# Performance work log

Measured on AMD Instinct MI355X. Metric: run time of the kernel, lower is better.

Reference implementation:

```python
import jax, jax.numpy as jnp
import numpy as np

B, C, H, W = 8, 64, 128, 128
NH, OPH = 4, 16
MX, MY = 32, 17  # n_modes=(32,32) -> modes_y = 32//2+1
NPAT_S, NPAT_F = 10000, 5000
ED_S, ED_F = 64, 32


def setup_inputs() -> dict:
    ks = jax.random.split(jax.random.key(0), 16)
    n = lambda k, s, sc=1.0: jax.random.normal(k, s, dtype=jnp.float32) * sc
    z = lambda s: jnp.zeros(s, jnp.float32)
    return dict(
        x=n(ks[0], (B, C, H, W)),
        se_emb=n(ks[1], (NPAT_S, ED_S)),
        se_w=n(ks[2], (ED_S, C), 0.1), se_b=z(C),
        mhf_wr=n(ks[3], (NH, C, OPH, MX, MY), 0.01),
        mhf_wi=n(ks[4], (NH, C, OPH, MX, MY), 0.01),
        mhf_bias=z(C),
        sp_emb=n(ks[5], (NPAT_F, ED_F)),
        sp_wr=n(ks[6], (ED_F, C * MX * MY), 0.05), sp_br=z(C * MX * MY),
        sp_wi=n(ks[7], (ED_F, C * MX * MY), 0.05), sp_bi=z(C * MX * MY),
        gate_w1=n(ks[8], (3 * C, 64), 0.05), gate_b1=z(64),
        gate_w2=n(ks[9], (64, 3), 0.05), gate_b2=z(3),
        skip_w=n(ks[10], (C, C), 0.05), skip_b=z(C),
        norm_g=jnp.ones(C), norm_b=z(C),
        mlp_w1=n(ks[11], (C, 2 * C), 0.05), mlp_b1=z(2 * C),
        mlp_w2=n(ks[12], (2 * C, C), 0.05), mlp_b2=z(C),
    )


def _gelu(v):
    return jax.nn.gelu(v, approximate=False)


def _block(x, se_emb, se_w, se_b, mhf_wr, mhf_wi, mhf_bias, sp_emb, sp_wr, sp_br,
           sp_wi, sp_bi, gate_w1, gate_b1, gate_w2, gate_b2, skip_w, skip_b,
           norm_g, norm_b, mlp_w1, mlp_b1, mlp_w2, mlp_b2):
    Bq, Cq, Hq, Wq = x.shape
    # --- SpatialEngram: quantization is elementwise, so sum over window entries
    # equals 3x3 box-sum of the quantized padded field (identical integers,
    # avoids materializing the (B,C,H,W,3,3) unfold tensor).
    xp = jnp.pad(x, ((0, 0), (0, 0), (1, 1), (1, 1)), mode='edge')
    q = (xp * 100.0).astype(jnp.int32)  # trunc toward zero, same as torch .long()
    hv = jnp.zeros((Bq, Cq, Hq, Wq), jnp.int32)
    for i in range(3):
        for j in range(3):
            hv = hv + q[:, :, i:i + Hq, j:j + Wq]
    idx = (jnp.abs(hv) % NPAT_S).astype(jnp.float32).mean(axis=1).astype(jnp.int32)  # (B,H,W)
    spatial = jnp.moveaxis(se_emb[idx] @ se_w + se_b, -1, 1)  # (B,C,H,W)
    # --- MHF multi-head spectral conv (all heads in one einsum; concat == reshape)
    xf = jnp.fft.rfft2(x, norm='ortho')          # (B,C,H,W//2+1) complex64
    lo = xf[:, :, :MX, :MY]
    wc = (mhf_wr + 1j * mhf_wi).astype(lo.dtype)
    of = jnp.einsum('biXY,hioXY->bhoXY', lo, wc).reshape(Bq, Cq, MX, MY)
    full = jnp.zeros((Bq, Cq, Hq, Wq // 2 + 1), lo.dtype).at[:, :, :MX, :MY].set(of)
    mhf = jnp.fft.irfft2(full, s=(Hq, Wq), norm='ortho') + mhf_bias[:, None, None]
    # --- SpectralEngram: per-sample hash of low-freq magnitude -> embedding -> freq proj
    mag = jnp.abs(lo).mean(axis=(1, 2, 3))                       # (B,)
    fidx = (mag * 1000.0).astype(jnp.int32) % NPAT_F
    fe = sp_emb[fidx]                                            # (B,ED_F)
    re = (fe @ sp_wr + sp_br).reshape(Bq, Cq, MX, MY)
    im = (fe @ sp_wi + sp_bi).reshape(Bq, Cq, MX, MY)
    full2 = jnp.zeros((Bq, Cq, Hq, Wq // 2 + 1), lo.dtype).at[:, :, :MX, :MY].set(re + 1j * im)
    spec = jnp.fft.irfft2(full2, s=(Hq, Wq), norm='ortho')
    # --- gated fusion
    gate_in = jnp.concatenate([spatial.mean((2, 3)), mhf.mean((2, 3)), spec.mean((2, 3))], axis=-1)
    gw = jax.nn.softmax(_gelu(gate_in @ gate_w1 + gate_b1) @ gate_w2 + gate_b2, axis=-1)
    a = gw[:, 0, None, None, None]
    bt = gw[:, 1, None, None, None]
    gm = gw[:, 2, None, None, None]
    fused = a * spatial + bt * mhf + gm * spec
    y = fused + jnp.einsum('bihw,io->bohw', x, skip_w) + skip_b[:, None, None]
    # --- GroupNorm(1,C) + 1x1-conv channel MLP (dropout=0)
    mu = y.mean((1, 2, 3), keepdims=True)
    var = y.var((1, 2, 3), keepdims=True)
    yn = (y - mu) * jax.lax.rsqrt(var + 1e-5) * norm_g[:, None, None] + norm_b[:, None, None]
    h = _gelu(jnp.einsum('bihw,io->bohw', yn, mlp_w1) + mlp_b1[:, None, None])
    h = jnp.einsum('bihw,io->bohw', h, mlp_w2) + mlp_b2[:, None, None]
    return y + h


def reference(x, se_emb, se_w, se_b, mhf_wr, mhf_wi, mhf_bias, sp_emb, sp_wr, sp_br,
              sp_wi, sp_bi, gate_w1, gate_b1, gate_w2, gate_b2, skip_w, skip_b,
              norm_g, norm_b, mlp_w1, mlp_b1, mlp_w2, mlp_b2):
    return _block(x, se_emb, se_w, se_b, mhf_wr, mhf_wi, mhf_bias, sp_emb, sp_wr, sp_br,
                  sp_wi, sp_bi, gate_w1, gate_b1, gate_w2, gate_b2, skip_w, skip_b,
                  norm_g, norm_b, mlp_w1, mlp_b1, mlp_w2, mlp_b2)
```

## Files before the change

kernel.cpp:

```cpp
#include <hip/hip_runtime.h>
#include <hip/hip_bf16.h>
#include <math.h>

#define B_ 8
#define C_ 64
#define H_ 128
#define W_ 128
#define NH_ 4
#define OPH_ 16
#define MX_ 32
#define MY_ 17
#define NPAT_F 5000
#define ED_F 32
#define XY_ (MX_*MY_)
#define HW_ (H_*W_)
#define NE_ (B_*C_*H_*W_)

#define OFF_LO     0u
#define OFF_T1     2228224u
#define OFF_T2     2228224u
#define OFF_FMHF   11141120u
#define OFF_FSPEC  13369344u
#define OFF_IDX    33030144u

typedef __hip_bfloat16 bf16;

template<typename T>
__device__ __forceinline__ float ldt(const void* p, int i){ return (float)(((const T*)p)[i]); }

template<typename T>
__device__ __forceinline__ float2 ld2(const void* p, int i){
  if(sizeof(T)==4) return *(const float2*)((const float*)p + i);
  unsigned raw = *(const unsigned*)((const unsigned short*)p + i);
  return make_float2(__uint_as_float(raw<<16), __uint_as_float(raw & 0xffff0000u));
}

__device__ __forceinline__ float gelu_f(float a){
  return 0.5f*a*(1.0f + erff(a*0.70710678118654752f));
}

__device__ __forceinline__ int detect_f32(const void* ng){
  return (((const unsigned*)ng)[0] == 0x3F800000u) ? 1 : 0;
}

template<typename T>
__device__ __forceinline__ void hash_body(const void* x, int* idx, int b, int h, int w){
  int hm = h>0 ? h-1 : 0, hp = h<127 ? h+1 : 127;
  int wm = w>0 ? w-1 : 0, wp = w<127 ? w+1 : 127;
  int s = 0;
  for(int c=0;c<C_;++c){
    const int base = ((b*C_+c)*H_)*W_;
    const int r0 = base + hm*W_, r1 = base + h*W_, r2 = base + hp*W_;
    int q = (int)(ldt<T>(x,r0+wm)*100.0f) + (int)(ldt<T>(x,r0+w)*100.0f) + (int)(ldt<T>(x,r0+wp)*100.0f)
          + (int)(ldt<T>(x,r1+wm)*100.0f) + (int)(ldt<T>(x,r1+w)*100.0f) + (int)(ldt<T>(x,r1+wp)*100.0f)
          + (int)(ldt<T>(x,r2+wm)*100.0f) + (int)(ldt<T>(x,r2+w)*100.0f) + (int)(ldt<T>(x,r2+wp)*100.0f);
    s += (q < 0 ? -q : q) % 10000;
  }
  idx[(b*H_+h)*W_+w] = s >> 6;
}

__global__ __launch_bounds__(256) void k_xprep(const void* __restrict__ x, double* __restrict__ t1,
                                               const void* ng, double* __restrict__ dmag,
                                               float* __restrict__ smean, int* __restrict__ idx){
  __shared__ float4 xs4[2048];
  __shared__ double2 csd[128];
  int t = threadIdx.x;
  int bid = blockIdx.x;
  int f = detect_f32(ng);
  if(bid == 0){
    if(t < 8) dmag[t] = 0.0;
    smean[t] = 0.f; smean[t+256] = 0.f;
  }
  if(bid < 1024){
    if(t<128){ double a = (double)t * (6.283185307179586476925286766559/128.0); csd[t] = make_double2(cos(a), sin(a)); }
    int h0 = (bid & 1) << 6, bcl = bid >> 1;
    long xbase = ((long)bcl*H_ + h0)*W_;
    if(f){
      const float4* xp = (const float4*)((const float*)x + xbase);
      for(int i=t;i<2048;i+=256){
        int r=i>>5, s=i&31;
        xs4[(r<<5) + (s ^ (r&31))] = xp[i];
      }
    } else {
      const uint2* xp = (const uint2*)((const unsigned short*)x + xbase);
      for(int i=t;i<2048;i+=256){
        int r=i>>5, s=i&31;
        uint2 raw = xp[i];
        xs4[(r<<5) + (s ^ (r&31))] = make_float4(
          __uint_as_float(raw.x<<16), __uint_as_float(raw.x & 0xffff0000u),
          __uint_as_float(raw.y<<16), __uint_as_float(raw.y & 0xffff0000u));
      }
    }
    __syncthreads();
    for(int o=t;o<MY_*64;o+=256){
      int ky = o>>6, hr = o&63;
      const float4* xr = xs4 + (hr<<5);
      const int sx = hr & 31;
      double ar=0.0, ai=0.0;
      int m = 0;
      for(int s=0;s<32;++s){
        float4 v4 = xr[s ^ sx];
        double2 c0 = csd[m]; ar = fma((double)v4.x, c0.x, ar); ai = fma(-(double)v4.x, c0.y, ai); m=(m+ky)&127;
        double2 c1 = csd[m]; ar = fma((double)v4.y, c1.x, ar); ai = fma(-(double)v4.y, c1.y, ai); m=(m+ky)&127;
        double2 c2 = csd[m]; ar = fma((double)v4.z, c2.x, ar); ai = fma(-(double)v4.z, c2.y, ai); m=(m+ky)&127;
        double2 c3 = csd[m]; ar = fma((double)v4.w, c3.x, ar); ai = fma(-(double)v4.w, c3.y, ai); m=(m+ky)&127;
      }
      long tt = ((long)(bcl*MY_ + ky))*H_ + (h0 + hr);
      *(double2*)(t1 + 2*tt) = make_double2(ar, ai);
    }
  } else {
    int hb = bid - 1024;
    int b = hb >> 6, h = ((hb & 63) << 1) + (t >> 7), w = t & 127;
    if(f) hash_body<float>(x, idx, b, h, w); else hash_body<bf16>(x, idx, b, h, w);
  }
}

__global__ __launch_bounds__(576) void k_f2m(const double* __restrict__ t1, float* __restrict__ lo,
                                             double* __restrict__ dmag){
  __shared__ double2 ts[MY_*129];
  __shared__ double2 csd[128];
  __shared__ double sred[9];
  int t = threadIdx.x;
  if(t<128){ double a = (double)t * (6.283185307179586476925286766559/128.0); csd[t] = make_double2(cos(a), sin(a)); }
  int bcl = blockIdx.x;
  const double2* tg = (const double2*)t1 + (size_t)bcl*MY_*H_;
  for(int i=t;i<MY_*H_;i+=576){ int ky=i>>7, hh=i&127; ts[ky*129+hh] = tg[i]; }
  __syncthreads();
  double s = 0.0;
  if(t < 544){
    int ky = t % MY_, kx = t / MY_;
    const double2* tr = ts + ky*129;
    double ar=0.0, ai=0.0;
    int m = 0;
    for(int h=0;h<H_;++h){
      double2 v = tr[h];
      double2 cs2 = csd[m];
      double vr = v.x, vi = v.y;
      double cc = cs2.x, ss = cs2.y;
      ar += vr*cc + vi*ss;
      ai += vi*cc - vr*ss;
      m = (m + kx) & 127;
    }
    int g = bcl*XY_ + kx*MY_ + ky;
    float fr = (float)(ar*(1.0/128.0)), fi = (float)(ai*(1.0/128.0));
    *(float2*)(lo + 2*g) = make_float2(fr, fi);
    double re = (double)fr, im = (double)fi;
    s = sqrt(re*re + im*im);
  }
  for(int off=32; off; off>>=1) s += __shfl_down(s, off);
  if((t & 63) == 0) sred[t >> 6] = s;
  __syncthreads();
  if(t == 0){
    double tot = 0.0;
    #pragma unroll
    for(int i=0;i<9;++i) tot += sred[i];
    atomicAdd(&dmag[bcl >> 6], tot);
  }
}

template<typename T>
__device__ __forceinline__ void spatial_load_w(const void* se_w, const void* se_b, float wsm[64][64], float* sb, int t){
  for(int i=t;i<4096;i+=256) wsm[i>>6][i&63] = ldt<T>(se_w, i);
  if(t<64) sb[t] = ldt<T>(se_b, t);
}
template<typename T>
__device__ __forceinline__ void spatial_load_emb(const void* se_emb, const int* ibs, float* emb, int w0, int t){
  for(int i=t;i<2048;i+=256){ int wl_=i>>6, e=i&63; emb[wl_*68 + e] = ldt<T>(se_emb, ibs[w0+wl_]*64 + e); }
}
__global__ __launch_bounds__(256) void k_spatial(const void* se_emb, const void* se_w, const void* se_b,
                                                 const int* __restrict__ idx, bf16* __restrict__ spatial,
                                                 float* __restrict__ smean, const void* ng){
  __shared__ float wsm[64][64];
  __shared__ float emb[32*68];
  __shared__ float sb[64];
  __shared__ int ibs[128];
  int b = blockIdx.x >> 7, h = blockIdx.x & 127, t = threadIdx.x;
  int f = detect_f32(ng);
  if(f) spatial_load_w<float>(se_w, se_b, wsm, sb, t); else spatial_load_w<bf16>(se_w, se_b, wsm, sb, t);
  if(t<128) ibs[t] = idx[(b*H_+h)*W_ + t];
  __syncthreads();
  const int tx = t & 15, ty = t >> 4;
  const int c0 = ty << 2;
  float gsum[4] = {0.f, 0.f, 0.f, 0.f};
  for(int chunk=0; chunk<4; ++chunk){
    int w0 = chunk*32;
    if(f) spatial_load_emb<float>(se_emb, ibs, emb, w0, t); else spatial_load_emb<bf16>(se_emb, ibs, emb, w0, t);
    __syncthreads();
    float acc0[4], acc1[4];
    #pragma unroll
    for(int j=0;j<4;++j){ acc0[j]=sb[c0+j]; acc1[j]=sb[c0+j]; }
    #pragma unroll
    for(int e=0;e<64;e+=4){
      float4 ea = *(const float4*)(emb + tx*68 + e);
      float4 eb = *(const float4*)(emb + (tx+16)*68 + e);
      float ea4[4] = {ea.x, ea.y, ea.z, ea.w};
      float eb4[4] = {eb.x, eb.y, eb.z, eb.w};
      #pragma unroll
      for(int d=0;d<4;++d){
        float4 wv = *(const float4*)(&wsm[e+d][c0]);
        float w4[4] = {wv.x, wv.y, wv.z, wv.w};
        #pragma unroll
        for(int j=0;j<4;++j){
          acc0[j] = fmaf(ea4[d], w4[j], acc0[j]);
          acc1[j] = fmaf(eb4[d], w4[j], acc1[j]);
        }
      }
    }
    #pragma unroll
    for(int j=0;j<4;++j){
      int cc = c0 + j;
      int gb = ((b*C_+cc)*H_+h)*W_ + w0;
      bf16 v0 = __float2bfloat16(acc0[j]);
      bf16 v1 = __float2bfloat16(acc1[j]);
      spatial[gb + tx]      = v0;
      spatial[gb + tx + 16] = v1;
      gsum[j] += __bfloat162float(v0) + __bfloat162float(v1);
    }
    __syncthreads();
  }
  #pragma unroll
  for(int j=0;j<4;++j){
    float g2 = gsum[j];
    g2 += __shfl_xor(g2, 1); g2 += __shfl_xor(g2, 2);
    g2 += __shfl_xor(g2, 4); g2 += __shfl_xor(g2, 8);
    if(tx == 0) atomicAdd(&smean[b*C_ + c0 + j], g2 * (1.0f/16384.0f));
  }
}

template<typename T>
__device__ __forceinline__ void mhf_body(const float* lp, const void* wr, const void* wi,
                                         float* fmhf, int b, int co){
  int hh = co >> 4, o = co & 15;
  for(int xy = threadIdx.x; xy < XY_; xy += 256){
    float ar=0.f, ai=0.f;
    for(int i=0;i<C_;++i){
      float2 l2 = *(const float2*)(lp + (i*XY_+xy)*2);
      float lr = l2.x, li = l2.y;
      int widx = ((hh*C_ + i)*OPH_ + o)*XY_ + xy;
      float wre = ldt<T>(wr, widx), wim = ldt<T>(wi, widx);
      ar += lr*wre - li*wim;
      ai += lr*wim + li*wre;
    }
    int oo = (b*C_ + co)*XY_ + xy;
    *(float2*)(fmhf + 2*oo) = make_float2(ar, ai);
  }
}
template<typename T>
__device__ __forceinline__ void specf_body(const void* sp_emb, const void* sp_wr, const void* sp_br,
                                           const void* sp_wi, const void* sp_bi, const double* dmag,
                                           float* fspec, float* fe, int b, int j0, int t){
  double mag = dmag[b] / (double)(C_*XY_);
  int fv = ((int)(mag*1000.0)) % NPAT_F;
  fv = fv < 0 ? 0 : (fv >= NPAT_F ? NPAT_F-1 : fv);
  if(t < ED_F) fe[t] = ldt<T>(sp_emb, fv*ED_F + t);
  __syncthreads();
  float2 rr = ld2<T>(sp_br, j0), ii = ld2<T>(sp_bi, j0);
  float re0=rr.x, re1=rr.y, im0=ii.x, im1=ii.y;
  #pragma unroll 8
  for(int e=0;e<ED_F;++e){
    float f = fe[e];
    float2 wr = ld2<T>(sp_wr, e*(C_*XY_)+j0);
    float2 wi = ld2<T>(sp_wi, e*(C_*XY_)+j0);
    re0 = fmaf(f, wr.x, re0); im0 = fmaf(f, wi.x, im0);
    re1 = fmaf(f, wr.y, re1); im1 = fmaf(f, wi.y, im1);
  }
  int o = b*C_*XY_ + j0;
  *(float4*)(fspec + 2*o) = make_float4(re0, im0, re1, im1);
}
__global__ __launch_bounds__(256) void k_msf(const float* __restrict__ lo, const void* wr, const void* wi,
                                             float* __restrict__ fmhf,
                                             const void* sp_emb, const void* sp_wr, const void* sp_br,
                                             const void* sp_wi, const void* sp_bi,
                                             const double* __restrict__ dmag,
                                             float* __restrict__ fspec, const void* ng){
  __shared__ float fe[ED_F];
  int bid = blockIdx.x;
  int f = detect_f32(ng);
  if(bid < 512){
    int xcd = bid & 7, slot = bid >> 3;
    int co = (xcd << 3) + (slot & 7);
    int b  = slot >> 3;
    const float* lp = lo + b*C_*XY_*2;
    if(f) mhf_body<float>(lp, wr, wi, fmhf, b, co); else mhf_body<bf16>(lp, wr, wi, fmhf, b, co);
  } else {
    int sidx = bid - 512;
    int b = sidx / 68;
    int j0 = ((sidx % 68)*256 + threadIdx.x)*2;
    if(f) specf_body<float>(sp_emb, sp_wr, sp_br, sp_wi, sp_bi, dmag, fspec, fe, b, j0, threadIdx.x);
    else  specf_body<bf16 >(sp_emb, sp_wr, sp_br, sp_wi, sp_bi, dmag, fspec, fe, b, j0, threadIdx.x);
  }
}

template<typename T>
__device__ __forceinline__ void gate_body(const float* smean, const float* fmhf, const float* fspec,
                                          const void* mbias, const void* w1, const void* b1,
                                          const void* w2, const void* b2,
                                          float* gw, float* ssum, float* ssq,
                                          float* gin, float* hid, int b, int t){
  gin[t]      = smean[b*C_+t];
  gin[64+t]   = fmhf [(b*C_+t)*XY_*2] * (1.0f/128.0f) + ldt<T>(mbias, t);
  gin[128+t]  = fspec[(b*C_+t)*XY_*2] * (1.0f/128.0f);
  __syncthreads();
  float acc = ldt<T>(b1, t);
  for(int k=0;k<192;++k) acc = fmaf(gin[k], ldt<T>(w1, k*64+t), acc);
  hid[t] = gelu_f(acc);
  __syncthreads();
  if(t==0){
    float o[3];
    for(int j=0;j<3;++j){
      float a = ldt<T>(b2, j);
      for(int k=0;k<64;++k) a += hid[k]*ldt<T>(w2, k*3+j);
      o[j]=a;
    }
    float mx = fmaxf(o[0], fmaxf(o[1], o[2]));
    float e0=expf(o[0]-mx), e1=expf(o[1]-mx), e2=expf(o[2]-mx);
    float sum=e0+e1+e2;
    gw[b*3+0]=e0/sum; gw[b*3+1]=e1/sum; gw[b*3+2]=e2/sum;
    ssum[b]=0.f; ssq[b]=0.f;
  }
}
__global__ __launch_bounds__(64) void k_gate(const float* __restrict__ smean, const float* __restrict__ fmhf,
                                             const float* __restrict__ fspec, const void* mbias,
                                             const void* w1, const void* b1, const void* w2, const void* b2,
                                             float* __restrict__ gw, float* __restrict__ ssum,
                                             float* __restrict__ ssq, const void* ng){
  __shared__ float gin[192];
  __shared__ float hid[64];
  int b = blockIdx.x, t = threadIdx.x;
  int f = detect_f32(ng);
  if(f) gate_body<float>(smean, fmhf, fspec, mbias, w1, b1, w2, b2, gw, ssum, ssq, gin, hid, b, t);
  else  gate_body<bf16 >(smean, fmhf, fspec, mbias, w1, b1, w2, b2, gw, ssum, ssq, gin, hid, b, t);
}

__global__ __launch_bounds__(256) void k_comb(const float* __restrict__ fmhf, const float* __restrict__ fspec,
                                              const float* __restrict__ gw, float* __restrict__ t2){
  __shared__ float Gr[XY_], Gi[XY_], cs[128], sn[128];
  int c = blockIdx.x, b = blockIdx.y, t = threadIdx.x;
  if(t<128) __sincosf((float)t * 0.04908738521234052f, &sn[t], &cs[t]);
  float bt=gw[b*3+1], gm=gw[b*3+2];
  for(int i=t;i<XY_;i+=256){
    int o = ((b*C_+c)*XY_+i)*2;
    float2 fm = *(const float2*)(fmhf + o);
    float2 fs = *(const float2*)(fspec + o);
    Gr[i] = bt*fm.x + gm*fs.x;
    Gi[i] = bt*fm.y + gm*fs.y;
  }
  __syncthreads();
  const int hh = t & 127;
  float cr[32], sr[32];
  #pragma unroll
  for(int kx=0;kx<MX_;++kx){ int m=(kx*hh)&127; cr[kx]=cs[m]; sr[kx]=sn[m]; }
  for(int i=t;i<MY_*H_;i+=256){
    int ky = i >> 7;
    float ar=0.f, ai=0.f;
    #pragma unroll 8
    for(int kx=0;kx<MX_;++kx){
      float fr=Gr[kx*MY_+ky], fi=Gi[kx*MY_+ky];
      ar += fr*cr[kx] - fi*sr[kx];
      ai += fr*sr[kx] + fi*cr[kx];
    }
    int e = (((b*C_+c)*MY_+ky)*H_ + hh)*2;
    *(float2*)(t2 + e) = make_float2(ar, ai);
  }
}

template<typename T>
__device__ __forceinline__ void fuse_body(const void* x, const void* skw, const void* skb, const void* mbias,
                                          bf16* sp_y, const float* t2, const float* gw,
                                          float* ssum, float* ssq,
                                          float wl[64][64], float Ur[64][17], float Ui[64][17],
                                          float* cs, float* sn, float* sb, float* mb,
                                          float* s1, float* s2, int b, int h, int t){
  int w = t & 127, half = t >> 7;
  if(t<128) __sincosf((float)t * 0.04908738521234052f, &sn[t], &cs[t]);
  for(int i=t;i<4096;i+=256) wl[i>>6][i&63] = ldt<T>(skw, i);
  if(t<64){ sb[t]=ldt<T>(skb,t); mb[t]=ldt<T>(mbias,t); }
  for(int i=t;i<C_*MY_;i+=256){
    int cc=i/MY_, ky=i%MY_;
    int e = (((b*C_+cc)*MY_+ky)*H_ + h)*2;
    float2 v = *(const float2*)(t2 + e);
    Ur[cc][ky]=v.x; Ui[cc][ky]=v.y;
  }
  float ga=gw[b*3], gbv=gw[b*3+1];
  __syncthreads();
  float cw[MY_], sw[MY_];
  #pragma unroll
  for(int ky=1;ky<MY_;++ky){ int m=(ky*w)&127; cw[ky]=cs[m]; sw[ky]=sn[m]; }
  int c0 = half*32;
  float acc[32];
  #pragma unroll
  for(int j=0;j<32;++j) acc[j]=sb[c0+j];
  int xb = (b*C_*H_ + h)*W_ + w;
  for(int k=0;k<64;++k){
    float xv = ldt<T>(x, xb + k*HW_);
    #pragma unroll
    for(int j=0;j<32;++j) acc[j] = fmaf(xv, wl[k][c0+j], acc[j]);
  }
  float ls=0.f, lq=0.f;
  for(int j=0;j<32;++j){
    int cc=c0+j;
    float vr = Ur[cc][0];
    #pragma unroll
    for(int ky=1;ky<MY_;++ky){
      vr += 2.0f*(Ur[cc][ky]*cw[ky] - Ui[cc][ky]*sw[ky]);
    }
    int gi = ((b*C_+cc)*H_+h)*W_+w;
    float v = ga*__bfloat162float(sp_y[gi]) + vr*(1.0f/128.0f) + gbv*mb[cc] + acc[j];
    sp_y[gi] = __float2bfloat16(v);
    ls += v; lq = fmaf(v, v, lq);
  }
  s1[t]=ls; s2[t]=lq; __syncthreads();
  for(int k=128;k>0;k>>=1){ if(t<k){ s1[t]+=s1[t+k]; s2[t]+=s2[t+k]; } __syncthreads(); }
  if(t==0){ atomicAdd(&ssum[b], s1[0]); atomicAdd(&ssq[b], s2[0]); }
}
__global__ __launch_bounds__(256) void k_fuse(const void* x, const void* skw, const void* skb, const void* mbias,
                                              bf16* __restrict__ sp_y, const float* __restrict__ t2,
                                              const float* __restrict__ gw,
                                              float* __restrict__ ssum, float* __restrict__ ssq, const void* ng){
  __shared__ float wl[64][64];
  __shared__ float Ur[64][17], Ui[64][17];
  __shared__ float cs[128], sn[128];
  __shared__ float sb[64], mb[64];
  __shared__ float s1[256], s2[256];
  int h = blockIdx.x, b = blockIdx.y, t = threadIdx.x;
  int f = detect_f32(ng);
  if(f) fuse_body<float>(x, skw, skb, mbias, sp_y, t2, gw, ssum, ssq, wl, Ur, Ui, cs, sn, sb, mb, s1, s2, b, h, t);
  else  fuse_body<bf16 >(x, skw, skb, mbias, sp_y, t2, gw, ssum, ssq, wl, Ur, Ui, cs, sn, sb, mb, s1, s2, b, h, t);
}

template<typename T>
__device__ __forceinline__ void mlp_body(const bf16* __restrict__ y, float mu, float rs,
                                         const void* ng, const void* nb, const void* w1, const void* b1,
                                         const void* w2, const void* b2, float* __restrict__ out,
                                         float* __restrict__ yn_s, float* __restrict__ w_s,
                                         int b, int h, int t){
  const int tx = t & 15, ty = t >> 4;
  const int pA = tx << 2, pB = 64 + (tx << 2);
  const int ybase = (b*C_*H_ + h)*W_;

  #pragma unroll
  for(int jj=0;jj<16;++jj) w_s[t + (jj<<8)] = ldt<T>(w1, t + (jj<<8));
  for(int it=0; it<8; ++it){
    int chunk = t + (it<<8);
    int c = chunk >> 5, p4 = (chunk & 31) << 2;
    const unsigned short* yp = (const unsigned short*)y + ybase + c*HW_ + p4;
    uint2 raw = *(const uint2*)yp;
    float g = ldt<T>(ng, c), nbv = ldt<T>(nb, c);
    float sc = rs*g;
    float4 o;
    o.x = (__uint_as_float(raw.x<<16)          - mu)*sc + nbv;
    o.y = (__uint_as_float(raw.x & 0xffff0000u)- mu)*sc + nbv;
    o.z = (__uint_as_float(raw.y<<16)          - mu)*sc + nbv;
    o.w = (__uint_as_float(raw.y & 0xffff0000u)- mu)*sc + nbv;
    *(float4*)(yn_s + c*132 + p4) = o;
  }
  float pf[16];
  #pragma unroll
  for(int jj=0;jj<16;++jj) pf[jj] = ldt<T>(w1, 4096 + t + (jj<<8));
  __syncthreads();

  const int kA = ty << 2, kB = 64 + (ty << 2);
  float a[8][8];
  #pragma unroll
  for(int j=0;j<4;++j){
    float bj = ldt<T>(b1, kA+j);
    float bj2 = ldt<T>(b1, kB+j);
    #pragma unroll
    for(int q=0;q<8;++q){ a[j][q]=bj; a[4+j][q]=bj2; }
  }
  #pragma unroll 4
  for(int i=0;i<32;++i){
    float4 y1 = *(const float4*)(yn_s + i*132 + pA);
    float4 y2 = *(const float4*)(yn_s + i*132 + pB);
    float4 wa = *(const float4*)(w_s + (i<<7) + kA);
    float4 wb = *(const float4*)(w_s + (i<<7) + kB);
    float y8[8] = {y1.x,y1.y,y1.z,y1.w,y2.x,y2.y,y2.z,y2.w};
    float w8[8] = {wa.x,wa.y,wa.z,wa.w,wb.x,wb.y,wb.z,wb.w};
    #pragma unroll
    for(int j=0;j<8;++j){
      #pragma unroll
      for(int q=0;q<8;++q) a[j][q] = fmaf(y8[q], w8[j], a[j][q]);
    }
  }
  __syncthreads();
  #pragma unroll
  for(int jj=0;jj<16;++jj) w_s[t + (jj<<8)] = pf[jj];
  #pragma unroll
  for(int jj=0;jj<16;++jj) pf[jj] = ldt<T>(w2, t + (jj<<8));
  __syncthreads();
  #pragma unroll 4
  for(int i=0;i<32;++i){
    float4 y1 = *(const float4*)(yn_s + (32+i)*132 + pA);
    float4 y2 = *(const float4*)(yn_s + (32+i)*132 + pB);
    float4 wa = *(const float4*)(w_s + (i<<7) + kA);
    float4 wb = *(const float4*)(w_s + (i<<7) + kB);
    float y8[8] = {y1.x,y1.y,y1.z,y1.w,y2.x,y2.y,y2.z,y2.w};
    float w8[8] = {wa.x,wa.y,wa.z,wa.w,wb.x,wb.y,wb.z,wb.w};
    #pragma unroll
    for(int j=0;j<8;++j){
      #pragma unroll
      for(int q=0;q<8;++q) a[j][q] = fmaf(y8[q], w8[j], a[j][q]);
    }
  }
  __syncthreads();
  #pragma unroll
  for(int jj=0;jj<16;++jj) w_s[t + (jj<<8)] = pf[jj];
  #pragma unroll
  for(int jj=0;jj<16;++jj) pf[jj] = ldt<T>(w2, 4096 + t + (jj<<8));
  #pragma unroll
  for(int j=0;j<4;++j){
    float4 h1, h2;
    h1.x = gelu_f(a[j][0]); h1.y = gelu_f(a[j][1]); h1.z = gelu_f(a[j][2]); h1.w = gelu_f(a[j][3]);
    h2.x = gelu_f(a[j][4]); h2.y = gelu_f(a[j][5]); h2.z = gelu_f(a[j][6]); h2.w = gelu_f(a[j][7]);
    *(float4*)(yn_s + (kA+j)*132 + pA) = h1;
    *(float4*)(yn_s + (kA+j)*132 + pB) = h2;
  }
  __syncthreads();

  const int c0 = ty << 2;
  float acc[4][8];
  #pragma unroll
  for(int j=0;j<4;++j){
    #pragma unroll
    for(int q=0;q<8;++q) acc[j][q] = 0.f;
  }
  #pragma unroll 4
  for(int k=0;k<64;++k){
    float4 h1 = *(const float4*)(yn_s + k*132 + pA);
    float4 h2 = *(const float4*)(yn_s + k*132 + pB);
    float4 wv = *(const float4*)(w_s + (k<<6) + c0);
    float h8[8] = {h1.x,h1.y,h1.z,h1.w,h2.x,h2.y,h2.z,h2.w};
    float w4[4] = {wv.x, wv.y, wv.z, wv.w};
    #pragma unroll
    for(int j=0;j<4;++j){
      #pragma unroll
      for(int q=0;q<8;++q) acc[j][q] = fmaf(h8[q], w4[j], acc[j][q]);
    }
  }
  __syncthreads();
  #pragma unroll
  for(int jj=0;jj<16;++jj) w_s[t + (jj<<8)] = pf[jj];
  #pragma unroll
  for(int j=0;j<4;++j){
    float4 h1, h2;
    h1.x = gelu_f(a[4+j][0]); h1.y = gelu_f(a[4+j][1]); h1.z = gelu_f(a[4+j][2]); h1.w = gelu_f(a[4+j][3]);
    h2.x = gelu_f(a[4+j][4]); h2.y = gelu_f(a[4+j][5]); h2.z = gelu_f(a[4+j][6]); h2.w = gelu_f(a[4+j][7]);
    *(float4*)(yn_s + (kA+j)*132 + pA) = h1;
    *(float4*)(yn_s + (kA+j)*132 + pB) = h2;
  }
  __syncthreads();
  #pragma unroll 4
  for(int k=0;k<64;++k){
    float4 h1 = *(const float4*)(yn_s + k*132 + pA);
    float4 h2 = *(const float4*)(yn_s + k*132 + pB);
    float4 wv = *(const float4*)(w_s + (k<<6) + c0);
    float h8[8] = {h1.x,h1.y,h1.z,h1.w,h2.x,h2.y,h2.z,h2.w};
    float w4[4] = {wv.x, wv.y, wv.z, wv.w};
    #pragma unroll
    for(int j=0;j<4;++j){
      #pragma unroll
      for(int q=0;q<8;++q) acc[j][q] = fmaf(h8[q], w4[j], acc[j][q]);
    }
  }

  #pragma unroll
  for(int j=0;j<4;++j){
    int c = c0 + j;
    float b2v = ldt<T>(b2, c);
    const unsigned short* yp1 = (const unsigned short*)y + ybase + c*HW_ + pA;
    const unsigned short* yp2 = (const unsigned short*)y + ybase + c*HW_ + pB;
    uint2 r1 = *(const uint2*)yp1;
    uint2 r2 = *(const uint2*)yp2;
    float4 o1, o2;
    o1.x = __uint_as_float(r1.x<<16)           + acc[j][0] + b2v;
    o1.y = __uint_as_float(r1.x & 0xffff0000u) + acc[j][1] + b2v;
    o1.z = __uint_as_float(r1.y<<16)           + acc[j][2] + b2v;
    o1.w = __uint_as_float(r1.y & 0xffff0000u) + acc[j][3] + b2v;
    o2.x = __uint_as_float(r2.x<<16)           + acc[j][4] + b2v;
    o2.y = __uint_as_float(r2.x & 0xffff0000u) + acc[j][5] + b2v;
    o2.z = __uint_as_float(r2.y<<16)           + acc[j][6] + b2v;
    o2.w = __uint_as_float(r2.y & 0xffff0000u) + acc[j][7] + b2v;
    *(float4*)(out + ybase + c*HW_ + pA) = o1;
    *(float4*)(out + ybase + c*HW_ + pB) = o2;
  }
}
__global__ __launch_bounds__(256) void k_mlp(const bf16* __restrict__ y, const float* __restrict__ ssum,
                                             const float* __restrict__ ssq, const void* ng, const void* nb,
                                             const void* w1, const void* b1, const void* w2, const void* b2,
                                             float* __restrict__ out){
  __shared__ float yn_s[64*132];
  __shared__ float w_s[4096];
  int h = blockIdx.x, b = blockIdx.y;
  int t = threadIdx.x;
  float m = ssum[b] * (1.0f/1048576.0f);
  float v = ssq[b] * (1.0f/1048576.0f) - m*m;
  float rs = rsqrtf(v + 1e-5f);
  int f = detect_f32(ng);
  if(f) mlp_body<float>(y, m, rs, ng, nb, w1, b1, w2, b2, out, yn_s, w_s, b, h, t);
  else  mlp_body<bf16 >(y, m, rs, ng, nb, w1, b1, w2, b2, out, yn_s, w_s, b, h, t);
}

extern "C" void kernel_launch(void* const* d_in, const int* in_sizes, int n_in,
                              void* d_out, int out_size, void* d_ws, size_t ws_size,
                              hipStream_t stream) {
  (void)out_size; (void)ws_size;
  static const int dict_sizes[24] = {8388608,640000,4096,64,2228224,2228224,64,160000,
                                     1114112,34816,1114112,34816,12288,64,192,3,
                                     4096,64,64,64,8192,128,8192,64};
  static const int sorted_sizes[24] = {64,3,12288,192,64,2228224,2228224,128,64,8192,8192,
                                       64,64,64,640000,4096,64,4096,34816,34816,160000,
                                       1114112,1114112,8388608};
  static const int sorted_to_dict[24] = {13,15,12,14,6,5,4,21,23,20,22,19,18,3,1,2,17,16,11,9,7,10,8,0};

  const void* in[24];
  bool is_dict = (n_in == 24), is_sorted = (n_in == 24);
  if(n_in == 24){
    for(int i=0;i<24;++i){
      if(in_sizes[i] != dict_sizes[i])   is_dict   = false;
      if(in_sizes[i] != sorted_sizes[i]) is_sorted = false;
    }
  }
  if(is_sorted && !is_dict){
    for(int i=0;i<24;++i) in[sorted_to_dict[i]] = d_in[i];
  } else {
    for(int i=0;i<24 && i<n_in;++i) in[i] = d_in[i];
  }

  const void* x       = in[0];
  const void* se_emb  = in[1];
  const void* se_w    = in[2];
  const void* se_b    = in[3];
  const void* mhf_wr  = in[4];
  const void* mhf_wi  = in[5];
  const void* mhf_bias= in[6];
  const void* sp_emb  = in[7];
  const void* sp_wr   = in[8];
  const void* sp_br   = in[9];
  const void* sp_wi   = in[10];
  const void* sp_bi   = in[11];
  const void* gate_w1 = in[12];
  const void* gate_b1 = in[13];
  const void* gate_w2 = in[14];
  const void* gate_b2 = in[15];
  const void* skip_w  = in[16];
  const void* skip_b  = in[17];
  const void* norm_g  = in[18];
  const void* norm_b  = in[19];
  const void* mlp_w1  = in[20];
  const void* mlp_b1  = in[21];
  const void* mlp_w2  = in[22];
  const void* mlp_b2  = in[23];
  float* out = (float*)d_out;

  bf16*   sp_y = (bf16*)d_ws;
  float*  scal = (float*)((char*)d_ws + (size_t)NE_*2);
  float* smean = scal;
  float* gw    = scal + 512;
  float* ssum  = scal + 536;
  float* ssq   = scal + 544;
  double* dmag = (double*)(scal + 584);

  char* ob = (char*)d_out;
  float*  lo    = (float*) (ob + OFF_LO);
  double* t1    = (double*)(ob + OFF_T1);
  float*  t2    = (float*) (ob + OFF_T2);
  float*  fmhf  = (float*) (ob + OFF_FMHF);
  float*  fspec = (float*) (ob + OFF_FSPEC);
  int*    idx   = (int*)   (ob + OFF_IDX);

  hipLaunchKernelGGL(k_xprep,  dim3(1536),       dim3(256), 0, stream, x, t1, norm_g, dmag, smean, idx);
  hipLaunchKernelGGL(k_f2m,    dim3(512),        dim3(576), 0, stream, t1, lo, dmag);
  hipLaunchKernelGGL(k_spatial,dim3(B_*H_),      dim3(256), 0, stream, se_emb, se_w, se_b, idx, sp_y, smean, norm_g);
  hipLaunchKernelGGL(k_msf,    dim3(1056),       dim3(256), 0, stream, lo, mhf_wr, mhf_wi, fmhf, sp_emb, sp_wr, sp_br, sp_wi, sp_bi, dmag, fspec, norm_g);
  hipLaunchKernelGGL(k_gate,   dim3(B_),         dim3(64),  0, stream, smean, fmhf, fspec, mhf_bias, gate_w1, gate_b1, gate_w2, gate_b2, gw, ssum, ssq, norm_g);
  hipLaunchKernelGGL(k_comb,   dim3(C_, B_),     dim3(256), 0, stream, fmhf, fspec, gw, t2);
  hipLaunchKernelGGL(k_fuse,   dim3(H_, B_),     dim3(256), 0, stream, x, skip_w, skip_b, mhf_bias, sp_y, t2, gw, ssum, ssq, norm_g);
  hipLaunchKernelGGL(k_mlp,    dim3(H_, B_),     dim3(256), 0, stream, sp_y, ssum, ssq, norm_g, norm_b, mlp_w1, mlp_b1, mlp_w2, mlp_b2, out);
}
```

Baseline: 423.0 us.

## Fold gate MLP into spectral combine kernel and vectorize fuse LDS reads

Removes the separate tiny k_gate launch. Each k_comb block now recomputes the gate MLP and softmax for its batch in shared memory, and block c==0 writes gw out for later kernels. The ssum/ssq zeroing moves into k_xprep. In k_fuse, the spectral coefficient arrays are re-laid out so the ky=0 term is separate and ky 1..16 sit in 16-wide rows, allowing float4 LDS reads. This trades one launch plus a serial dependency for 64x redundant gate computation per batch.

```diff
diff --git a/kernel.cpp b/kernel.cpp
--- a/kernel.cpp
+++ b/kernel.cpp
@@ -61,14 +61,15 @@
 
 __global__ __launch_bounds__(256) void k_xprep(const void* __restrict__ x, double* __restrict__ t1,
                                                const void* ng, double* __restrict__ dmag,
-                                               float* __restrict__ smean, int* __restrict__ idx){
+                                               float* __restrict__ smean, float* __restrict__ ssum,
+                                               float* __restrict__ ssq, int* __restrict__ idx){
   __shared__ float4 xs4[2048];
   __shared__ double2 csd[128];
   int t = threadIdx.x;
   int bid = blockIdx.x;
   int f = detect_f32(ng);
   if(bid == 0){
-    if(t < 8) dmag[t] = 0.0;
+    if(t < 8){ dmag[t] = 0.0; ssum[t] = 0.f; ssq[t] = 0.f; }
     smean[t] = 0.f; smean[t+256] = 0.f;
   }
   if(bid < 1024){
@@ -292,18 +293,21 @@
 }
 
 template<typename T>
-__device__ __forceinline__ void gate_body(const float* smean, const float* fmhf, const float* fspec,
+__device__ __forceinline__ void gate_calc(const float* smean, const float* fmhf, const float* fspec,
                                           const void* mbias, const void* w1, const void* b1,
                                           const void* w2, const void* b2,
-                                          float* gw, float* ssum, float* ssq,
-                                          float* gin, float* hid, int b, int t){
-  gin[t]      = smean[b*C_+t];
-  gin[64+t]   = fmhf [(b*C_+t)*XY_*2] * (1.0f/128.0f) + ldt<T>(mbias, t);
-  gin[128+t]  = fspec[(b*C_+t)*XY_*2] * (1.0f/128.0f);
-  __syncthreads();
-  float acc = ldt<T>(b1, t);
-  for(int k=0;k<192;++k) acc = fmaf(gin[k], ldt<T>(w1, k*64+t), acc);
-  hid[t] = gelu_f(acc);
+                                          float* gin, float* hid, float* gwsh, int b, int t){
+  if(t < 64){
+    gin[t]      = smean[b*C_+t];
+    gin[64+t]   = fmhf [(b*C_+t)*XY_*2] * (1.0f/128.0f) + ldt<T>(mbias, t);
+    gin[128+t]  = fspec[(b*C_+t)*XY_*2] * (1.0f/128.0f);
+  }
+  __syncthreads();
+  if(t < 64){
+    float acc = ldt<T>(b1, t);
+    for(int k=0;k<192;++k) acc = fmaf(gin[k], ldt<T>(w1, k*64+t), acc);
+    hid[t] = gelu_f(acc);
+  }
   __syncthreads();
   if(t==0){
     float o[3];
@@ -315,29 +319,25 @@
     float mx = fmaxf(o[0], fmaxf(o[1], o[2]));
     float e0=expf(o[0]-mx), e1=expf(o[1]-mx), e2=expf(o[2]-mx);
     float sum=e0+e1+e2;
-    gw[b*3+0]=e0/sum; gw[b*3+1]=e1/sum; gw[b*3+2]=e2/sum;
-    ssum[b]=0.f; ssq[b]=0.f;
-  }
-}
-__global__ __launch_bounds__(64) void k_gate(const float* __restrict__ smean, const float* __restrict__ fmhf,
-                                             const float* __restrict__ fspec, const void* mbias,
-                                             const void* w1, const void* b1, const void* w2, const void* b2,
-                                             float* __restrict__ gw, float* __restrict__ ssum,
-                                             float* __restrict__ ssq, const void* ng){
+    gwsh[0]=e0/sum; gwsh[1]=e1/sum; gwsh[2]=e2/sum;
+  }
+}
+__global__ __launch_bounds__(256) void k_comb(const float* __restrict__ fmhf, const float* __restrict__ fspec,
+                                              const float* __restrict__ smean, const void* mbias,
+                                              const void* gw1, const void* gb1, const void* gw2, const void* gb2,
+                                              float* __restrict__ gw, float* __restrict__ t2, const void* ng){
+  __shared__ float Gr[XY_], Gi[XY_], cs[128], sn[128];
   __shared__ float gin[192];
   __shared__ float hid[64];
-  int b = blockIdx.x, t = threadIdx.x;
+  __shared__ float gwsh[3];
+  int c = blockIdx.x, b = blockIdx.y, t = threadIdx.x;
   int f = detect_f32(ng);
-  if(f) gate_body<float>(smean, fmhf, fspec, mbias, w1, b1, w2, b2, gw, ssum, ssq, gin, hid, b, t);
-  else  gate_body<bf16 >(smean, fmhf, fspec, mbias, w1, b1, w2, b2, gw, ssum, ssq, gin, hid, b, t);
-}
-
-__global__ __launch_bounds__(256) void k_comb(const float* __restrict__ fmhf, const float* __restrict__ fspec,
-                                              const float* __restrict__ gw, float* __restrict__ t2){
-  __shared__ float Gr[XY_], Gi[XY_], cs[128], sn[128];
-  int c = blockIdx.x, b = blockIdx.y, t = threadIdx.x;
   if(t<128) __sincosf((float)t * 0.04908738521234052f, &sn[t], &cs[t]);
-  float bt=gw[b*3+1], gm=gw[b*3+2];
+  if(f) gate_calc<float>(smean, fmhf, fspec, mbias, gw1, gb1, gw2, gb2, gin, hid, gwsh, b, t);
+  else  gate_calc<bf16 >(smean, fmhf, fspec, mbias, gw1, gb1, gw2, gb2, gin, hid, gwsh, b, t);
+  __syncthreads();
+  float bt=gwsh[1], gm=gwsh[2];
+  if(c==0 && t<3) gw[b*3+t] = gwsh[t];
   for(int i=t;i<XY_;i+=256){
     int o = ((b*C_+c)*XY_+i)*2;
     float2 fm = *(const float2*)(fmhf + o);
@@ -368,7 +368,7 @@
 __device__ __forceinline__ void fuse_body(const void* x, const void* skw, const void* skb, const void* mbias,
                                           bf16* sp_y, const float* t2, const float* gw,
                                           float* ssum, float* ssq,
-                                          float wl[64][64], float Ur[64][17], float Ui[64][17],
+                                          float wl[64][64], float* Ur0, float (*UrT)[16], float (*UiT)[16],
                                           float* cs, float* sn, float* sb, float* mb,
                                           float* s1, float* s2, int b, int h, int t){
   int w = t & 127, half = t >> 7;
@@ -379,7 +379,8 @@
     int cc=i/MY_, ky=i%MY_;
     int e = (((b*C_+cc)*MY_+ky)*H_ + h)*2;
     float2 v = *(const float2*)(t2 + e);
-    Ur[cc][ky]=v.x; Ui[cc][ky]=v.y;
+    if(ky==0){ Ur0[cc]=v.x; }
+    else { UrT[cc][ky-1]=v.x; UiT[cc][ky-1]=v.y; }
   }
   float ga=gw[b*3], gbv=gw[b*3+1];
   __syncthreads();
@@ -399,11 +400,31 @@
   float ls=0.f, lq=0.f;
   for(int j=0;j<32;++j){
     int cc=c0+j;
-    float vr = Ur[cc][0];
-    #pragma unroll
-    for(int ky=1;ky<MY_;++ky){
-      vr += 2.0f*(Ur[cc][ky]*cw[ky] - Ui[cc][ky]*sw[ky]);
-    }
+    float vr = Ur0[cc];
+    float4 ur0 = *(const float4*)(&UrT[cc][0]);
+    float4 ur1 = *(const float4*)(&UrT[cc][4]);
+    float4 ur2 = *(const float4*)(&UrT[cc][8]);
+    float4 ur3 = *(const float4*)(&UrT[cc][12]);
+    float4 ui0 = *(const float4*)(&UiT[cc][0]);
+    float4 ui1 = *(const float4*)(&UiT[cc][4]);
+    float4 ui2 = *(const float4*)(&UiT[cc][8]);
+    float4 ui3 = *(const float4*)(&UiT[cc][12]);
+    vr += 2.0f*(ur0.x*cw[1]  - ui0.x*sw[1]);
+    vr += 2.0f*(ur0.y*cw[2]  - ui0.y*sw[2]);
+    vr += 2.0f*(ur0.z*cw[3]  - ui0.z*sw[3]);
+    vr += 2.0f*(ur0.w*cw[4]  - ui0.w*sw[4]);
+    vr += 2.0f*(ur1.x*cw[5]  - ui1.x*sw[5]);
+    vr += 2.0f*(ur1.y*cw[6]  - ui1.y*sw[6]);
+    vr += 2.0f*(ur1.z*cw[7]  - ui1.z*sw[7]);
+    vr += 2.0f*(ur1.w*cw[8]  - ui1.w*sw[8]);
+    vr += 2.0f*(ur2.x*cw[9]  - ui2.x*sw[9]);
+    vr += 2.0f*(ur2.y*cw[10] - ui2.y*sw[10]);
+    vr += 2.0f*(ur2.z*cw[11] - ui2.z*sw[11]);
+    vr += 2.0f*(ur2.w*cw[12] - ui2.w*sw[12]);
+    vr += 2.0f*(ur3.x*cw[13] - ui3.x*sw[13]);
+    vr += 2.0f*(ur3.y*cw[14] - ui3.y*sw[14]);
+    vr += 2.0f*(ur3.z*cw[15] - ui3.z*sw[15]);
+    vr += 2.0f*(ur3.w*cw[16] - ui3.w*sw[16]);
     int gi = ((b*C_+cc)*H_+h)*W_+w;
     float v = ga*__bfloat162float(sp_y[gi]) + vr*(1.0f/128.0f) + gbv*mb[cc] + acc[j];
     sp_y[gi] = __float2bfloat16(v);
@@ -418,14 +439,15 @@
                                               const float* __restrict__ gw,
                                               float* __restrict__ ssum, float* __restrict__ ssq, const void* ng){
   __shared__ float wl[64][64];
-  __shared__ float Ur[64][17], Ui[64][17];
+  __shared__ float Ur0[64];
+  __shared__ float UrT[64][16], UiT[64][16];
   __shared__ float cs[128], sn[128];
   __shared__ float sb[64], mb[64];
   __shared__ float s1[256], s2[256];
   int h = blockIdx.x, b = blockIdx.y, t = threadIdx.x;
   int f = detect_f32(ng);
-  if(f) fuse_body<float>(x, skw, skb, mbias, sp_y, t2, gw, ssum, ssq, wl, Ur, Ui, cs, sn, sb, mb, s1, s2, b, h, t);
-  else  fuse_body<bf16 >(x, skw, skb, mbias, sp_y, t2, gw, ssum, ssq, wl, Ur, Ui, cs, sn, sb, mb, s1, s2, b, h, t);
+  if(f) fuse_body<float>(x, skw, skb, mbias, sp_y, t2, gw, ssum, ssq, wl, Ur0, UrT, UiT, cs, sn, sb, mb, s1, s2, b, h, t);
+  else  fuse_body<bf16 >(x, skw, skb, mbias, sp_y, t2, gw, ssum, ssq, wl, Ur0, UrT, UiT, cs, sn, sb, mb, s1, s2, b, h, t);
 }
 
 template<typename T>
@@ -668,12 +690,11 @@
   float*  fspec = (float*) (ob + OFF_FSPEC);
   int*    idx   = (int*)   (ob + OFF_IDX);
 
-  hipLaunchKernelGGL(k_xprep,  dim3(1536),       dim3(256), 0, stream, x, t1, norm_g, dmag, smean, idx);
+  hipLaunchKernelGGL(k_xprep,  dim3(1536),       dim3(256), 0, stream, x, t1, norm_g, dmag, smean, ssum, ssq, idx);
   hipLaunchKernelGGL(k_f2m,    dim3(512),        dim3(576), 0, stream, t1, lo, dmag);
   hipLaunchKernelGGL(k_spatial,dim3(B_*H_),      dim3(256), 0, stream, se_emb, se_w, se_b, idx, sp_y, smean, norm_g);
   hipLaunchKernelGGL(k_msf,    dim3(1056),       dim3(256), 0, stream, lo, mhf_wr, mhf_wi, fmhf, sp_emb, sp_wr, sp_br, sp_wi, sp_bi, dmag, fspec, norm_g);
-  hipLaunchKernelGGL(k_gate,   dim3(B_),         dim3(64),  0, stream, smean, fmhf, fspec, mhf_bias, gate_w1, gate_b1, gate_w2, gate_b2, gw, ssum, ssq, norm_g);
-  hipLaunchKernelGGL(k_comb,   dim3(C_, B_),     dim3(256), 0, stream, fmhf, fspec, gw, t2);
+  hipLaunchKernelGGL(k_comb,   dim3(C_, B_),     dim3(256), 0, stream, fmhf, fspec, smean, mhf_bias, gate_w1, gate_b1, gate_w2, gate_b2, gw, t2, norm_g);
   hipLaunchKernelGGL(k_fuse,   dim3(H_, B_),     dim3(256), 0, stream, x, skip_w, skip_b, mhf_bias, sp_y, t2, gw, ssum, ssq, norm_g);
   hipLaunchKernelGGL(k_mlp,    dim3(H_, B_),     dim3(256), 0, stream, sp_y, ssum, ssq, norm_g, norm_b, mlp_w1, mlp_b1, mlp_w2, mlp_b2, out);
 }
```

Result: slower. 434.0 us (+2.6%).
